# Optimization experiments

Measured on AMD Instinct MI355X. Metric: run time of the kernel, lower is better.

## Reference

```python
import jax, jax.numpy as jnp
import numpy as np
import math

EMB, HEADS, LATENT, FFN = 1024, 16, 256, 4096
HEAD_DIM = EMB // HEADS
B, N = 2, 2048
EPS = 1e-5


def _layer_norm(x, g, b):
    m = jnp.mean(x, axis=-1, keepdims=True)
    v = jnp.mean(jnp.square(x - m), axis=-1, keepdims=True)
    return (x - m) * jax.lax.rsqrt(v + EPS) * g + b


def setup_inputs() -> dict:
    key = jax.random.key(0)
    ks = jax.random.split(key, 20)
    s = 0.02
    def w(k, shape):
        return jax.random.normal(k, shape, dtype=jnp.float32) * s
    return {
        "x": jax.random.normal(ks[0], (B, N, EMB), dtype=jnp.float32),
        "attn_bias": jax.random.normal(ks[1], (N, N), dtype=jnp.float32),
        "Wq_w": w(ks[2], (EMB, EMB)),   "Wq_b": jnp.zeros((EMB,), jnp.float32),
        "WaK_w": w(ks[3], (EMB, LATENT)), "WaK_b": jnp.zeros((LATENT,), jnp.float32),
        "WbK_w": w(ks[4], (LATENT, EMB)), "WbK_b": jnp.zeros((EMB,), jnp.float32),
        "WaV_w": w(ks[5], (EMB, LATENT)), "WaV_b": jnp.zeros((LATENT,), jnp.float32),
        "WbV_w": w(ks[6], (LATENT, EMB)), "WbV_b": jnp.zeros((EMB,), jnp.float32),
        "Wo_w": w(ks[7], (EMB, EMB)),   "Wo_b": jnp.zeros((EMB,), jnp.float32),
        "ffn1_w": w(ks[8], (EMB, FFN)), "ffn1_b": jnp.zeros((FFN,), jnp.float32),
        "ffn2_w": w(ks[9], (FFN, EMB)), "ffn2_b": jnp.zeros((EMB,), jnp.float32),
        "ln1_g": jnp.ones((EMB,), jnp.float32), "ln1_b": jnp.zeros((EMB,), jnp.float32),
        "ln2_g": jnp.ones((EMB,), jnp.float32), "ln2_b": jnp.zeros((EMB,), jnp.float32),
    }


def reference(x, attn_bias, Wq_w, Wq_b, WaK_w, WaK_b, WbK_w, WbK_b,
              WaV_w, WaV_b, WbV_w, WbV_b, Wo_w, Wo_b,
              ffn1_w, ffn1_b, ffn2_w, ffn2_b, ln1_g, ln1_b, ln2_g, ln2_b):
    b, n, _ = x.shape
    Q = x @ Wq_w + Wq_b                                   # [B,N,E]
    K = (x @ WaK_w + WaK_b) @ WbK_w + WbK_b               # low-rank K
    V = (x @ WaV_w + WaV_b) @ WbV_w + WbV_b               # low-rank V
    Qh = Q.reshape(b, n, HEADS, HEAD_DIM)
    Kh = K.reshape(b, n, HEADS, HEAD_DIM)
    Vh = V.reshape(b, n, HEADS, HEAD_DIM)
    scale = 1.0 / math.sqrt(HEAD_DIM)
    scores = jnp.einsum('bnhd,bmhd->bhnm', Qh, Kh) * scale
    scores = scores + attn_bias[None, None, :, :]
    weights = jax.nn.softmax(scores, axis=-1)
    O = jnp.einsum('bhnm,bmhd->bnhd', weights, Vh).reshape(b, n, EMB)
    O = O @ Wo_w + Wo_b
    x1 = _layer_norm(x + O, ln1_g, ln1_b)
    h = jax.nn.gelu(x1 @ ffn1_w + ffn1_b, approximate=False)
    ffn_out = h @ ffn2_w + ffn2_b
    return _layer_norm(x1 + ffn_out, ln2_g, ln2_b)
```

## Files before the change

### kernel.cpp

```cpp
#include <hip/hip_runtime.h>
#include <hip/hip_bf16.h>
#include <math.h>

typedef __attribute__((ext_vector_type(4))) float f32x4;
typedef __attribute__((ext_vector_type(8))) __bf16 bf16x8;
typedef unsigned short u16;

#define L2E 1.44269504088896f

__device__ __forceinline__ u16 f2b(float f) {
  union { float f; unsigned u; } x; x.f = f;
  unsigned r = x.u + 0x7fffu + ((x.u >> 16) & 1u);
  return (u16)(r >> 16);
}

__device__ __forceinline__ void gl_lds16(const void* g, void* l) {
  __builtin_amdgcn_global_load_lds(
      (const __attribute__((address_space(1))) void*)g,
      (__attribute__((address_space(3))) void*)l, 16, 0, 0);
}

template<int EPI, int BN, int SPLITK>
__global__ __launch_bounds__(256, 3)
void gemm_bt(const u16* __restrict__ A, int lda,
             const u16* __restrict__ Bt,
             const float* __restrict__ bias,
             void* __restrict__ C, void* __restrict__ C2, int ldc,
             int M, int N, int K)
{
  constexpr int NF = BN / 32;
  __shared__ u16 As[128 * 32];
  __shared__ u16 Bs[BN * 32];
  const int t = threadIdx.x;
  const int lane = t & 63;
  const int w = t >> 6;
  const int wr = w >> 1, wc = w & 1;
  const int row0 = blockIdx.y * 128, col0 = blockIdx.x * BN;
  const int r = lane & 15, g = lane >> 4;

  f32x4 acc[4][NF];
#pragma unroll
  for (int m = 0; m < 4; ++m)
#pragma unroll
    for (int n = 0; n < NF; ++n) acc[m][n] = (f32x4){0.f, 0.f, 0.f, 0.f};

  const int KS = K / SPLITK;
  const int kbeg = (SPLITK > 1) ? blockIdx.z * KS : 0;

  const u16* Ag = A + (size_t)(row0 + (t >> 2)) * lda + (t & 3) * 8 + kbeg;
  const u16* Bg = Bt + (size_t)(col0 + (t >> 2)) * K + (t & 3) * 8 + kbeg;
  u16* Asw  = &As[t * 8];
  u16* Asw2 = &As[(t + 256) * 8];
  u16* Bsw  = &Bs[t * 8];
  u16* Bsw2 = (BN == 128) ? &Bs[(t + 256) * 8] : nullptr;
  const size_t a2 = (size_t)64 * lda, bo2 = (size_t)64 * K;

  for (int kt = 0; kt < KS; kt += 32) {
    gl_lds16(Ag + kt, Asw);
    gl_lds16(Ag + a2 + kt, Asw2);
    gl_lds16(Bg + kt, Bsw);
    if constexpr (BN == 128) gl_lds16(Bg + bo2 + kt, Bsw2);
    __syncthreads();
    bf16x8 af[4], bfr[NF];
#pragma unroll
    for (int m = 0; m < 4; ++m)
      af[m] = *(const bf16x8*)&As[(wr * 64 + m * 16 + r) * 32 + g * 8];
#pragma unroll
    for (int n = 0; n < NF; ++n)
      bfr[n] = *(const bf16x8*)&Bs[(wc * (BN / 2) + n * 16 + r) * 32 + g * 8];
#pragma unroll
    for (int m = 0; m < 4; ++m)
#pragma unroll
      for (int n = 0; n < NF; ++n)
        acc[m][n] = __builtin_amdgcn_mfma_f32_16x16x32_bf16(af[m], bfr[n], acc[m][n], 0, 0, 0);
    __syncthreads();
  }

  bool addb = true;
  float* Cf = (float*)C;
  if constexpr (SPLITK > 1) {
    if (blockIdx.z != 0) { addb = false; Cf = (float*)C2; }
  }

#pragma unroll
  for (int n = 0; n < NF; ++n) {
    const int col = col0 + wc * (BN / 2) + n * 16 + r;
    const float bv = addb ? bias[col] : 0.f;
#pragma unroll
    for (int m = 0; m < 4; ++m) {
      const int rb = row0 + wr * 64 + m * 16 + g * 4;
      if constexpr (EPI == 3) {
        const int b_ = rb >> 11, nn = rb & 2047;
        const int h_ = col >> 6, d_ = col & 63;
        u16* vp = (u16*)C + ((size_t)((b_ * 16 + h_) * 64 + d_)) * 2048 + nn;
        ushort4 pk;
        pk.x = f2b(acc[m][n][0] + bv);
        pk.y = f2b(acc[m][n][1] + bv);
        pk.z = f2b(acc[m][n][2] + bv);
        pk.w = f2b(acc[m][n][3] + bv);
        *(ushort4*)vp = pk;
      } else {
#pragma unroll
        for (int j = 0; j < 4; ++j) {
          float v = acc[m][n][j] + bv;
          if constexpr (EPI == 1) v = 0.5f * v * (1.0f + erff(v * 0.70710678118654752f));
          const size_t idx = (size_t)(rb + j) * ldc + col;
          if constexpr (EPI == 2) Cf[idx] = v;
          else ((u16*)C)[idx] = f2b(v);
        }
      }
    }
  }
}

__global__ __launch_bounds__(256, 4)
void attn_kernel(const u16* __restrict__ Qg,
                 const u16* __restrict__ Kg,
                 const u16* __restrict__ Vt,
                 const float* __restrict__ Bf,
                 u16* __restrict__ O)
{
  const int bh = blockIdx.x;
  const int b = bh >> 4, h = bh & 15;
  const int q0 = blockIdx.y * 64;
  const int t = threadIdx.x;
  const int lane = t & 63;
  const int w = t >> 6;
  const int r = lane & 15, g = lane >> 4;

  __shared__ u16 Ks[64 * 64];
  __shared__ u16 Vs[64 * 64];
  __shared__ __bf16 Ps[4][16 * 64];

  bf16x8 qa[2];
  {
    const size_t qrow = (size_t)(b * 2048 + q0 + w * 16 + r);
    const u16* qp = Qg + qrow * 1536 + h * 64 + g * 8;
    qa[0] = *(const bf16x8*)qp;
    qa[1] = *(const bf16x8*)(qp + 32);
#pragma unroll
    for (int dh = 0; dh < 2; ++dh)
#pragma unroll
      for (int i = 0; i < 8; ++i)
        qa[dh][i] = (__bf16)((float)qa[dh][i] * (0.125f * L2E));
  }

  f32x4 Oa[4];
#pragma unroll
  for (int dc = 0; dc < 4; ++dc) Oa[dc] = (f32x4){0.f, 0.f, 0.f, 0.f};
  float lsum[4] = {0.f, 0.f, 0.f, 0.f};

  const int srow = t >> 3;
  const int spos = t & 7;
  const int sseg  = spos ^ (srow & 7);
  const int srow2 = srow + 32;
  const int sseg2 = spos ^ (srow2 & 7);

  const float* bp = Bf + (size_t)(q0 + w * 16 + g * 4) * 2048 + r;

  for (int mt = 0; mt < 32; ++mt) {
    const int m0 = mt * 64;
    gl_lds16(Kg + (size_t)(b * 2048 + m0 + srow)  * 1024 + h * 64 + sseg * 8,  &Ks[t * 8]);
    gl_lds16(Kg + (size_t)(b * 2048 + m0 + srow2) * 1024 + h * 64 + sseg2 * 8, &Ks[(t + 256) * 8]);
    gl_lds16(Vt + (size_t)(bh * 64 + srow)  * 2048 + m0 + sseg * 8,  &Vs[t * 8]);
    gl_lds16(Vt + (size_t)(bh * 64 + srow2) * 2048 + m0 + sseg2 * 8, &Vs[(t + 256) * 8]);

    f32x4 s[4];
#pragma unroll
    for (int mc = 0; mc < 4; ++mc)
#pragma unroll
      for (int j = 0; j < 4; ++j)
        s[mc][j] = bp[(size_t)j * 2048 + m0 + mc * 16] * L2E;

    __syncthreads();

#pragma unroll
    for (int mc = 0; mc < 4; ++mc) {
      const int mrow = mc * 16 + r;
      const bf16x8 kb0 = *(const bf16x8*)&Ks[mrow * 64 + (((0 * 4 + g) ^ (mrow & 7)) * 8)];
      const bf16x8 kb1 = *(const bf16x8*)&Ks[mrow * 64 + (((1 * 4 + g) ^ (mrow & 7)) * 8)];
      s[mc] = __builtin_amdgcn_mfma_f32_16x16x32_bf16(qa[0], kb0, s[mc], 0, 0, 0);
      s[mc] = __builtin_amdgcn_mfma_f32_16x16x32_bf16(qa[1], kb1, s[mc], 0, 0, 0);
    }

    __bf16* pw = (__bf16*)Ps[w];
#pragma unroll
    for (int mc = 0; mc < 4; ++mc) {
      const int mm = mc * 16 + r;
#pragma unroll
      for (int j = 0; j < 4; ++j) {
        const float p = __builtin_amdgcn_exp2f(s[mc][j]);
        lsum[j] += p;
        const int qr = g * 4 + j;
        pw[qr * 64 + (((mm >> 3) ^ (qr & 7)) * 8) + (mm & 7)] = (__bf16)p;
      }
    }

    const bf16x8 pa0 = *(const bf16x8*)&pw[r * 64 + (((0 * 4 + g) ^ (r & 7)) * 8)];
    const bf16x8 pa1 = *(const bf16x8*)&pw[r * 64 + (((1 * 4 + g) ^ (r & 7)) * 8)];
#pragma unroll
    for (int dc = 0; dc < 4; ++dc) {
      const int drow = dc * 16 + r;
      const bf16x8 vb0 = *(const bf16x8*)&Vs[drow * 64 + (((0 * 4 + g) ^ (drow & 7)) * 8)];
      const bf16x8 vb1 = *(const bf16x8*)&Vs[drow * 64 + (((1 * 4 + g) ^ (drow & 7)) * 8)];
      Oa[dc] = __builtin_amdgcn_mfma_f32_16x16x32_bf16(pa0, vb0, Oa[dc], 0, 0, 0);
      Oa[dc] = __builtin_amdgcn_mfma_f32_16x16x32_bf16(pa1, vb1, Oa[dc], 0, 0, 0);
    }
    __syncthreads();
  }

#pragma unroll
  for (int off = 1; off < 16; off <<= 1)
#pragma unroll
    for (int j = 0; j < 4; ++j) lsum[j] += __shfl_xor(lsum[j], off);

  u16* Os = Ks;
#pragma unroll
  for (int j = 0; j < 4; ++j) {
    const float inv = 1.0f / lsum[j];
    const int qr = w * 16 + g * 4 + j;
#pragma unroll
    for (int dc = 0; dc < 4; ++dc)
      Os[qr * 64 + dc * 16 + r] = f2b(Oa[dc][j] * inv);
  }
  __syncthreads();
#pragma unroll
  for (int i = 0; i < 2; ++i) {
    const int tt = t + i * 256;
    const int orow = tt >> 3, oseg = tt & 7;
    const uint4 v = *(const uint4*)&Os[orow * 64 + oseg * 8];
    *(uint4*)&O[(size_t)(b * 2048 + q0 + orow) * 1024 + h * 64 + oseg * 8] = v;
  }
}

__global__ __launch_bounds__(256)
void prep_weights(const float* __restrict__ Wq, const float* __restrict__ WaK,
                  const float* __restrict__ WaV, const float* __restrict__ WbK,
                  const float* __restrict__ WbV, const float* __restrict__ Wo,
                  const float* __restrict__ F1, const float* __restrict__ F2,
                  u16* __restrict__ WB1, u16* __restrict__ WbKT,
                  u16* __restrict__ WbVT, u16* __restrict__ WoT,
                  u16* __restrict__ F1T, u16* __restrict__ F2T)
{
  const int bid = blockIdx.x;
  const float* src; u16* dst; int R, C, tile, tilesX;
  if (bid < 1024)      { src = Wq;  dst = WB1;             R = 1024; C = 1024; tile = bid;        tilesX = 32; }
  else if (bid < 1280) { src = WaK; dst = WB1 + 1024*1024; R = 1024; C = 256;  tile = bid - 1024; tilesX = 8; }
  else if (bid < 1536) { src = WaV; dst = WB1 + 1280*1024; R = 1024; C = 256;  tile = bid - 1280; tilesX = 8; }
  else if (bid < 1792) { src = WbK; dst = WbKT;            R = 256;  C = 1024; tile = bid - 1536; tilesX = 32; }
  else if (bid < 2048) { src = WbV; dst = WbVT;            R = 256;  C = 1024; tile = bid - 1792; tilesX = 32; }
  else if (bid < 3072) { src = Wo;  dst = WoT;             R = 1024; C = 1024; tile = bid - 2048; tilesX = 32; }
  else if (bid < 7168) { src = F1;  dst = F1T;             R = 1024; C = 4096; tile = bid - 3072; tilesX = 128; }
  else                 { src = F2;  dst = F2T;             R = 4096; C = 1024; tile = bid - 7168; tilesX = 32; }
  const int bx = tile % tilesX, by = tile / tilesX;
  const int c0 = bx * 32, r0 = by * 32;

  __shared__ float tl[32][33];
  const int tx = threadIdx.x, ty = threadIdx.y;
#pragma unroll
  for (int i = 0; i < 4; ++i)
    tl[ty + i * 8][tx] = src[(size_t)(r0 + ty + i * 8) * C + c0 + tx];
  __syncthreads();
#pragma unroll
  for (int i = 0; i < 4; ++i)
    dst[(size_t)(c0 + ty + i * 8) * R + r0 + tx] = f2b(tl[tx][ty + i * 8]);
}

__global__ void cvt_f32_bf16(const float* __restrict__ in, u16* __restrict__ out, int n4)
{
  const int i = blockIdx.x * 256 + threadIdx.x;
  if (i >= n4) return;
  const float4 v = ((const float4*)in)[i];
  ushort4 o;
  o.x = f2b(v.x); o.y = f2b(v.y); o.z = f2b(v.z); o.w = f2b(v.w);
  ((ushort4*)out)[i] = o;
}

__global__ void concat_bias(const float* __restrict__ a, const float* __restrict__ b,
                            const float* __restrict__ c, float* __restrict__ o)
{
  const int i = blockIdx.x * 256 + threadIdx.x;
  if (i < 1024) o[i] = a[i];
  else if (i < 1280) o[i] = b[i - 1024];
  else if (i < 1536) o[i] = c[i - 1280];
}

template<int WB, int NP>
__global__ __launch_bounds__(256)
void ln_kernel(const float* __restrict__ xa, const float* __restrict__ y0,
               const float* __restrict__ y1,
               const float* __restrict__ gam, const float* __restrict__ bet,
               float* __restrict__ outf, u16* __restrict__ outb)
{
  const int row = blockIdx.x, t = threadIdx.x;
  const float4 a = ((const float4*)(xa + (size_t)row * 1024))[t];
  const float4 c = ((const float4*)(y0 + (size_t)row * 1024))[t];
  float v0 = a.x + c.x, v1 = a.y + c.y, v2 = a.z + c.z, v3 = a.w + c.w;
  if constexpr (NP == 2) {
    const float4 d = ((const float4*)(y1 + (size_t)row * 1024))[t];
    v0 += d.x; v1 += d.y; v2 += d.z; v3 += d.w;
  }
  float s = v0 + v1 + v2 + v3;
  float q = v0 * v0 + v1 * v1 + v2 * v2 + v3 * v3;
#pragma unroll
  for (int off = 1; off < 64; off <<= 1) {
    s += __shfl_xor(s, off);
    q += __shfl_xor(q, off);
  }
  __shared__ float ss[4], qs[4];
  const int w = t >> 6, lane = t & 63;
  if (lane == 0) { ss[w] = s; qs[w] = q; }
  __syncthreads();
  const float S = ss[0] + ss[1] + ss[2] + ss[3];
  const float Q = qs[0] + qs[1] + qs[2] + qs[3];
  const float mean = S * (1.0f / 1024.0f);
  const float var = Q * (1.0f / 1024.0f) - mean * mean;
  const float rstd = rsqrtf(var + 1e-5f);
  const float4 gm = ((const float4*)gam)[t];
  const float4 bt = ((const float4*)bet)[t];
  const float o0 = (v0 - mean) * rstd * gm.x + bt.x;
  const float o1 = (v1 - mean) * rstd * gm.y + bt.y;
  const float o2 = (v2 - mean) * rstd * gm.z + bt.z;
  const float o3 = (v3 - mean) * rstd * gm.w + bt.w;
  float4 ov; ov.x = o0; ov.y = o1; ov.z = o2; ov.w = o3;
  ((float4*)(outf + (size_t)row * 1024))[t] = ov;
  if constexpr (WB) {
    ushort4 ob; ob.x = f2b(o0); ob.y = f2b(o1); ob.z = f2b(o2); ob.w = f2b(o3);
    ((ushort4*)(outb + (size_t)row * 1024))[t] = ob;
  }
}

extern "C" void kernel_launch(void* const* d_in, const int* in_sizes, int n_in,
                              void* d_out, int out_size, void* d_ws, size_t ws_size,
                              hipStream_t stream)
{
  const float* x     = (const float*)d_in[0];
  const float* abias = (const float*)d_in[1];
  const float* Wq_w  = (const float*)d_in[2];
  const float* Wq_b  = (const float*)d_in[3];
  const float* WaK_w = (const float*)d_in[4];
  const float* WaK_b = (const float*)d_in[5];
  const float* WbK_w = (const float*)d_in[6];
  const float* WbK_b = (const float*)d_in[7];
  const float* WaV_w = (const float*)d_in[8];
  const float* WaV_b = (const float*)d_in[9];
  const float* WbV_w = (const float*)d_in[10];
  const float* WbV_b = (const float*)d_in[11];
  const float* Wo_w  = (const float*)d_in[12];
  const float* Wo_b  = (const float*)d_in[13];
  const float* f1_w  = (const float*)d_in[14];
  const float* f1_b  = (const float*)d_in[15];
  const float* f2_w  = (const float*)d_in[16];
  const float* f2_b  = (const float*)d_in[17];
  const float* ln1_g = (const float*)d_in[18];
  const float* ln1_b = (const float*)d_in[19];
  const float* ln2_g = (const float*)d_in[20];
  const float* ln2_b = (const float*)d_in[21];

  char* ws = (char*)d_ws;
  u16*   xb    = (u16*)(ws + 0);
  u16*   WB1   = (u16*)(ws + 8388608);
  u16*   WbKT  = (u16*)(ws + 11534336);
  u16*   WbVT  = (u16*)(ws + 12058624);
  u16*   WoT   = (u16*)(ws + 12582912);
  u16*   F1T   = (u16*)(ws + 14680064);
  u16*   F2T   = (u16*)(ws + 23068672);
  float* bias1 = (float*)(ws + 31457280);
  u16*   G1    = (u16*)(ws + 39854080);
  u16*   Kb    = (u16*)(ws + 52436992);
  u16*   Vt    = (u16*)(ws + 60825600);
  u16*   Ob    = (u16*)(ws + 69214208);
  float* Y     = (float*)(ws + 77602816);
  float* x1f   = (float*)(ws + 94380032);
  u16*   x1b   = (u16*)(ws + 111157248);
  u16*   hbuf  = G1;
  float* Y1    = (float*)(ws + 0);

  prep_weights<<<11264, dim3(32, 8), 0, stream>>>(Wq_w, WaK_w, WaV_w, WbK_w, WbV_w,
                                                  Wo_w, f1_w, f2_w,
                                                  WB1, WbKT, WbVT, WoT, F1T, F2T);
  cvt_f32_bf16<<<4096, 256, 0, stream>>>(x, xb, 1048576);
  concat_bias<<<6, 256, 0, stream>>>(Wq_b, WaK_b, WaV_b, bias1);

  gemm_bt<0, 128, 1><<<dim3(12, 32), 256, 0, stream>>>(xb, 1024, WB1, bias1, G1, nullptr, 1536, 4096, 1536, 1024);
  gemm_bt<0, 64, 1><<<dim3(16, 32), 256, 0, stream>>>(G1 + 1024, 1536, WbKT, WbK_b, Kb, nullptr, 1024, 4096, 1024, 256);
  gemm_bt<3, 64, 1><<<dim3(16, 32), 256, 0, stream>>>(G1 + 1280, 1536, WbVT, WbV_b, Vt, nullptr, 2048, 4096, 1024, 256);
  attn_kernel<<<dim3(32, 32), 256, 0, stream>>>(G1, Kb, Vt, abias, Ob);
  gemm_bt<2, 64, 1><<<dim3(16, 32), 256, 0, stream>>>(Ob, 1024, WoT, Wo_b, Y, nullptr, 1024, 4096, 1024, 1024);
  ln_kernel<1, 1><<<4096, 256, 0, stream>>>(x, Y, Y, ln1_g, ln1_b, x1f, x1b);
  gemm_bt<1, 128, 1><<<dim3(32, 32), 256, 0, stream>>>(x1b, 1024, F1T, f1_b, hbuf, nullptr, 4096, 4096, 4096, 1024);
  gemm_bt<2, 128, 2><<<dim3(8, 32, 2), 256, 0, stream>>>(hbuf, 4096, F2T, f2_b, Y, Y1, 1024, 4096, 1024, 4096);
  ln_kernel<0, 2><<<4096, 256, 0, stream>>>(x1f, Y, Y1, ln2_g, ln2_b, (float*)d_out, nullptr);
}
```

Before: 417.7 us.

## Shrink attention blocks, prefetch bias tile into registers, raise MFMA priority

The attention kernel now runs 128-thread blocks that each cover 32 query rows, so the grid has twice as many blocks and more of them can be resident for latency hiding. The attn_bias values for the next key tile are loaded into registers during the current iteration instead of just before the QK MFMAs. s_setprio is raised around the MFMA sections. In exchange, every K/V tile is fetched into LDS by twice as many blocks, which raises global/L2 traffic and the per-block staging overhead.

Measured after the change: 425.4 us. No clear change (+1.8%).

```diff
diff --git a/kernel.cpp b/kernel.cpp
--- a/kernel.cpp
+++ b/kernel.cpp
@@ -113,7 +113,7 @@
   }
 }
 
-__global__ __launch_bounds__(256, 4)
+__global__ __launch_bounds__(128, 4)
 void attn_kernel(const u16* __restrict__ Qg,
                  const u16* __restrict__ Kg,
                  const u16* __restrict__ Vt,
@@ -122,7 +122,7 @@
 {
   const int bh = blockIdx.x;
   const int b = bh >> 4, h = bh & 15;
-  const int q0 = blockIdx.y * 64;
+  const int q0 = blockIdx.y * 32;
   const int t = threadIdx.x;
   const int lane = t & 63;
   const int w = t >> 6;
@@ -130,7 +130,7 @@
 
   __shared__ u16 Ks[64 * 64];
   __shared__ u16 Vs[64 * 64];
-  __shared__ __bf16 Ps[4][16 * 64];
+  __shared__ __bf16 Ps[2][16 * 64];
 
   bf16x8 qa[2];
   {
@@ -150,30 +150,48 @@
   for (int dc = 0; dc < 4; ++dc) Oa[dc] = (f32x4){0.f, 0.f, 0.f, 0.f};
   float lsum[4] = {0.f, 0.f, 0.f, 0.f};
 
-  const int srow = t >> 3;
-  const int spos = t & 7;
-  const int sseg  = spos ^ (srow & 7);
-  const int srow2 = srow + 32;
-  const int sseg2 = spos ^ (srow2 & 7);
+  int srw[4], ssg[4];
+#pragma unroll
+  for (int i = 0; i < 4; ++i) {
+    const int s_ = i * 128 + t;
+    srw[i] = s_ >> 3;
+    ssg[i] = (s_ & 7) ^ (srw[i] & 7);
+  }
+  const u16* Kb4[4];
+  const u16* Vb4[4];
+#pragma unroll
+  for (int i = 0; i < 4; ++i) {
+    Kb4[i] = Kg + (size_t)(b * 2048 + srw[i]) * 1024 + h * 64 + ssg[i] * 8;
+    Vb4[i] = Vt + (size_t)(bh * 64 + srw[i]) * 2048 + ssg[i] * 8;
+  }
 
   const float* bp = Bf + (size_t)(q0 + w * 16 + g * 4) * 2048 + r;
+
+  float bn[4][4];
+#pragma unroll
+  for (int mc = 0; mc < 4; ++mc)
+#pragma unroll
+    for (int j = 0; j < 4; ++j)
+      bn[mc][j] = bp[(size_t)j * 2048 + mc * 16];
 
   for (int mt = 0; mt < 32; ++mt) {
     const int m0 = mt * 64;
-    gl_lds16(Kg + (size_t)(b * 2048 + m0 + srow)  * 1024 + h * 64 + sseg * 8,  &Ks[t * 8]);
-    gl_lds16(Kg + (size_t)(b * 2048 + m0 + srow2) * 1024 + h * 64 + sseg2 * 8, &Ks[(t + 256) * 8]);
-    gl_lds16(Vt + (size_t)(bh * 64 + srow)  * 2048 + m0 + sseg * 8,  &Vs[t * 8]);
-    gl_lds16(Vt + (size_t)(bh * 64 + srow2) * 2048 + m0 + sseg2 * 8, &Vs[(t + 256) * 8]);
+#pragma unroll
+    for (int i = 0; i < 4; ++i) {
+      gl_lds16(Kb4[i] + (size_t)m0 * 1024, &Ks[(i * 128 + t) * 8]);
+      gl_lds16(Vb4[i] + m0, &Vs[(i * 128 + t) * 8]);
+    }
 
     f32x4 s[4];
 #pragma unroll
     for (int mc = 0; mc < 4; ++mc)
 #pragma unroll
       for (int j = 0; j < 4; ++j)
-        s[mc][j] = bp[(size_t)j * 2048 + m0 + mc * 16] * L2E;
+        s[mc][j] = bn[mc][j] * L2E;
 
     __syncthreads();
 
+    __builtin_amdgcn_s_setprio(1);
 #pragma unroll
     for (int mc = 0; mc < 4; ++mc) {
       const int mrow = mc * 16 + r;
@@ -182,6 +200,15 @@
       s[mc] = __builtin_amdgcn_mfma_f32_16x16x32_bf16(qa[0], kb0, s[mc], 0, 0, 0);
       s[mc] = __builtin_amdgcn_mfma_f32_16x16x32_bf16(qa[1], kb1, s[mc], 0, 0, 0);
     }
+    __builtin_amdgcn_s_setprio(0);
+
+    if (mt < 31) {
+#pragma unroll
+      for (int mc = 0; mc < 4; ++mc)
+#pragma unroll
+        for (int j = 0; j < 4; ++j)
+          bn[mc][j] = bp[(size_t)j * 2048 + (m0 + 64) + mc * 16];
+    }
 
     __bf16* pw = (__bf16*)Ps[w];
 #pragma unroll
@@ -198,6 +225,7 @@
 
     const bf16x8 pa0 = *(const bf16x8*)&pw[r * 64 + (((0 * 4 + g) ^ (r & 7)) * 8)];
     const bf16x8 pa1 = *(const bf16x8*)&pw[r * 64 + (((1 * 4 + g) ^ (r & 7)) * 8)];
+    __builtin_amdgcn_s_setprio(1);
 #pragma unroll
     for (int dc = 0; dc < 4; ++dc) {
       const int drow = dc * 16 + r;
@@ -206,6 +234,7 @@
       Oa[dc] = __builtin_amdgcn_mfma_f32_16x16x32_bf16(pa0, vb0, Oa[dc], 0, 0, 0);
       Oa[dc] = __builtin_amdgcn_mfma_f32_16x16x32_bf16(pa1, vb1, Oa[dc], 0, 0, 0);
     }
+    __builtin_amdgcn_s_setprio(0);
     __syncthreads();
   }
 
@@ -226,7 +255,7 @@
   __syncthreads();
 #pragma unroll
   for (int i = 0; i < 2; ++i) {
-    const int tt = t + i * 256;
+    const int tt = t + i * 128;
     const int orow = tt >> 3, oseg = tt & 7;
     const uint4 v = *(const uint4*)&Os[orow * 64 + oseg * 8];
     *(uint4*)&O[(size_t)(b * 2048 + q0 + orow) * 1024 + h * 64 + oseg * 8] = v;
@@ -385,7 +414,7 @@
   gemm_bt<0, 128, 1><<<dim3(12, 32), 256, 0, stream>>>(xb, 1024, WB1, bias1, G1, nullptr, 1536, 4096, 1536, 1024);
   gemm_bt<0, 64, 1><<<dim3(16, 32), 256, 0, stream>>>(G1 + 1024, 1536, WbKT, WbK_b, Kb, nullptr, 1024, 4096, 1024, 256);
   gemm_bt<3, 64, 1><<<dim3(16, 32), 256, 0, stream>>>(G1 + 1280, 1536, WbVT, WbV_b, Vt, nullptr, 2048, 4096, 1024, 256);
-  attn_kernel<<<dim3(32, 32), 256, 0, stream>>>(G1, Kb, Vt, abias, Ob);
+  attn_kernel<<<dim3(32, 64), 128, 0, stream>>>(G1, Kb, Vt, abias, Ob);
   gemm_bt<2, 64, 1><<<dim3(16, 32), 256, 0, stream>>>(Ob, 1024, WoT, Wo_b, Y, nullptr, 1024, 4096, 1024, 1024);
   ln_kernel<1, 1><<<4096, 256, 0, stream>>>(x, Y, Y, ln1_g, ln1_b, x1f, x1b);
   gemm_bt<1, 128, 1><<<dim3(32, 32), 256, 0, stream>>>(x1b, 1024, F1T, f1_b, hbuf, nullptr, 4096, 4096, 4096, 1024);
```

## Double-buffer LDS tiles in GEMM and attention loops, prefetch bias, raise MFMA priority

Applied to the files above, without the earlier changes.

Both the GEMM and the attention kernels now keep two LDS buffers. The loads for the next K or KV tile are issued before computing on the current one, so each iteration has one barrier instead of stalling on a load before every compute step. The attention kernel also loads the next tile's bias values into registers during the current iteration. MFMA sections are wrapped in s_setprio. LDS use per block doubles for the K/V and A/B tiles, which may limit occupancy. This matters most for the attention kernel, which is already near the LDS limit at 4 blocks per CU.

Result: no change. 418.2 us (+0.1%).

```diff
diff --git a/kernel.cpp b/kernel.cpp
--- a/kernel.cpp
+++ b/kernel.cpp
@@ -29,8 +29,8 @@
              int M, int N, int K)
 {
   constexpr int NF = BN / 32;
-  __shared__ u16 As[128 * 32];
-  __shared__ u16 Bs[BN * 32];
+  __shared__ u16 As[2][128 * 32];
+  __shared__ u16 Bs[2][BN * 32];
   const int t = threadIdx.x;
   const int lane = t & 63;
   const int w = t >> 6;
@@ -49,31 +49,40 @@
 
   const u16* Ag = A + (size_t)(row0 + (t >> 2)) * lda + (t & 3) * 8 + kbeg;
   const u16* Bg = Bt + (size_t)(col0 + (t >> 2)) * K + (t & 3) * 8 + kbeg;
-  u16* Asw  = &As[t * 8];
-  u16* Asw2 = &As[(t + 256) * 8];
-  u16* Bsw  = &Bs[t * 8];
-  u16* Bsw2 = (BN == 128) ? &Bs[(t + 256) * 8] : nullptr;
   const size_t a2 = (size_t)64 * lda, bo2 = (size_t)64 * K;
-
+  const int si0 = t * 8, si1 = (t + 256) * 8;
+
+  gl_lds16(Ag, &As[0][si0]);
+  gl_lds16(Ag + a2, &As[0][si1]);
+  gl_lds16(Bg, &Bs[0][si0]);
+  if constexpr (BN == 128) gl_lds16(Bg + bo2, &Bs[0][si1]);
+  __syncthreads();
+
+  int buf = 0;
   for (int kt = 0; kt < KS; kt += 32) {
-    gl_lds16(Ag + kt, Asw);
-    gl_lds16(Ag + a2 + kt, Asw2);
-    gl_lds16(Bg + kt, Bsw);
-    if constexpr (BN == 128) gl_lds16(Bg + bo2 + kt, Bsw2);
-    __syncthreads();
+    const int kn = kt + 32;
+    if (kn < KS) {
+      gl_lds16(Ag + kn, &As[buf ^ 1][si0]);
+      gl_lds16(Ag + a2 + kn, &As[buf ^ 1][si1]);
+      gl_lds16(Bg + kn, &Bs[buf ^ 1][si0]);
+      if constexpr (BN == 128) gl_lds16(Bg + bo2 + kn, &Bs[buf ^ 1][si1]);
+    }
     bf16x8 af[4], bfr[NF];
 #pragma unroll
     for (int m = 0; m < 4; ++m)
-      af[m] = *(const bf16x8*)&As[(wr * 64 + m * 16 + r) * 32 + g * 8];
+      af[m] = *(const bf16x8*)&As[buf][(wr * 64 + m * 16 + r) * 32 + g * 8];
 #pragma unroll
     for (int n = 0; n < NF; ++n)
-      bfr[n] = *(const bf16x8*)&Bs[(wc * (BN / 2) + n * 16 + r) * 32 + g * 8];
+      bfr[n] = *(const bf16x8*)&Bs[buf][(wc * (BN / 2) + n * 16 + r) * 32 + g * 8];
+    __builtin_amdgcn_s_setprio(1);
 #pragma unroll
     for (int m = 0; m < 4; ++m)
 #pragma unroll
       for (int n = 0; n < NF; ++n)
         acc[m][n] = __builtin_amdgcn_mfma_f32_16x16x32_bf16(af[m], bfr[n], acc[m][n], 0, 0, 0);
+    __builtin_amdgcn_s_setprio(0);
     __syncthreads();
+    buf ^= 1;
   }
 
   bool addb = true;
@@ -128,8 +137,8 @@
   const int w = t >> 6;
   const int r = lane & 15, g = lane >> 4;
 
-  __shared__ u16 Ks[64 * 64];
-  __shared__ u16 Vs[64 * 64];
+  __shared__ u16 Ks[2][64 * 64];
+  __shared__ u16 Vs[2][64 * 64];
   __shared__ __bf16 Ps[4][16 * 64];
 
   bf16x8 qa[2];
@@ -155,32 +164,63 @@
   const int sseg  = spos ^ (srow & 7);
   const int srow2 = srow + 32;
   const int sseg2 = spos ^ (srow2 & 7);
+  const int si0 = t * 8, si1 = (t + 256) * 8;
+
+  const u16* Kp0 = Kg + (size_t)(b * 2048 + srow)  * 1024 + h * 64 + sseg * 8;
+  const u16* Kp1 = Kg + (size_t)(b * 2048 + srow2) * 1024 + h * 64 + sseg2 * 8;
+  const u16* Vp0 = Vt + (size_t)(bh * 64 + srow)  * 2048 + sseg * 8;
+  const u16* Vp1 = Vt + (size_t)(bh * 64 + srow2) * 2048 + sseg2 * 8;
 
   const float* bp = Bf + (size_t)(q0 + w * 16 + g * 4) * 2048 + r;
 
+  float bn[4][4];
+#pragma unroll
+  for (int mc = 0; mc < 4; ++mc)
+#pragma unroll
+    for (int j = 0; j < 4; ++j)
+      bn[mc][j] = bp[(size_t)j * 2048 + mc * 16];
+
+  gl_lds16(Kp0, &Ks[0][si0]);
+  gl_lds16(Kp1, &Ks[0][si1]);
+  gl_lds16(Vp0, &Vs[0][si0]);
+  gl_lds16(Vp1, &Vs[0][si1]);
+  __syncthreads();
+
+  int buf = 0;
   for (int mt = 0; mt < 32; ++mt) {
     const int m0 = mt * 64;
-    gl_lds16(Kg + (size_t)(b * 2048 + m0 + srow)  * 1024 + h * 64 + sseg * 8,  &Ks[t * 8]);
-    gl_lds16(Kg + (size_t)(b * 2048 + m0 + srow2) * 1024 + h * 64 + sseg2 * 8, &Ks[(t + 256) * 8]);
-    gl_lds16(Vt + (size_t)(bh * 64 + srow)  * 2048 + m0 + sseg * 8,  &Vs[t * 8]);
-    gl_lds16(Vt + (size_t)(bh * 64 + srow2) * 2048 + m0 + sseg2 * 8, &Vs[(t + 256) * 8]);
+    if (mt < 31) {
+      const int mn = m0 + 64;
+      gl_lds16(Kp0 + (size_t)mn * 1024, &Ks[buf ^ 1][si0]);
+      gl_lds16(Kp1 + (size_t)mn * 1024, &Ks[buf ^ 1][si1]);
+      gl_lds16(Vp0 + mn, &Vs[buf ^ 1][si0]);
+      gl_lds16(Vp1 + mn, &Vs[buf ^ 1][si1]);
+    }
 
     f32x4 s[4];
 #pragma unroll
     for (int mc = 0; mc < 4; ++mc)
 #pragma unroll
       for (int j = 0; j < 4; ++j)
-        s[mc][j] = bp[(size_t)j * 2048 + m0 + mc * 16] * L2E;
-
-    __syncthreads();
-
+        s[mc][j] = bn[mc][j] * L2E;
+
+    __builtin_amdgcn_s_setprio(1);
 #pragma unroll
     for (int mc = 0; mc < 4; ++mc) {
       const int mrow = mc * 16 + r;
-      const bf16x8 kb0 = *(const bf16x8*)&Ks[mrow * 64 + (((0 * 4 + g) ^ (mrow & 7)) * 8)];
-      const bf16x8 kb1 = *(const bf16x8*)&Ks[mrow * 64 + (((1 * 4 + g) ^ (mrow & 7)) * 8)];
+      const bf16x8 kb0 = *(const bf16x8*)&Ks[buf][mrow * 64 + (((0 * 4 + g) ^ (mrow & 7)) * 8)];
+      const bf16x8 kb1 = *(const bf16x8*)&Ks[buf][mrow * 64 + (((1 * 4 + g) ^ (mrow & 7)) * 8)];
       s[mc] = __builtin_amdgcn_mfma_f32_16x16x32_bf16(qa[0], kb0, s[mc], 0, 0, 0);
       s[mc] = __builtin_amdgcn_mfma_f32_16x16x32_bf16(qa[1], kb1, s[mc], 0, 0, 0);
+    }
+    __builtin_amdgcn_s_setprio(0);
+
+    if (mt < 31) {
+#pragma unroll
+      for (int mc = 0; mc < 4; ++mc)
+#pragma unroll
+        for (int j = 0; j < 4; ++j)
+          bn[mc][j] = bp[(size_t)j * 2048 + (m0 + 64) + mc * 16];
     }
 
     __bf16* pw = (__bf16*)Ps[w];
@@ -198,15 +238,18 @@
 
     const bf16x8 pa0 = *(const bf16x8*)&pw[r * 64 + (((0 * 4 + g) ^ (r & 7)) * 8)];
     const bf16x8 pa1 = *(const bf16x8*)&pw[r * 64 + (((1 * 4 + g) ^ (r & 7)) * 8)];
+    __builtin_amdgcn_s_setprio(1);
 #pragma unroll
     for (int dc = 0; dc < 4; ++dc) {
       const int drow = dc * 16 + r;
-      const bf16x8 vb0 = *(const bf16x8*)&Vs[drow * 64 + (((0 * 4 + g) ^ (drow & 7)) * 8)];
-      const bf16x8 vb1 = *(const bf16x8*)&Vs[drow * 64 + (((1 * 4 + g) ^ (drow & 7)) * 8)];
+      const bf16x8 vb0 = *(const bf16x8*)&Vs[buf][drow * 64 + (((0 * 4 + g) ^ (drow & 7)) * 8)];
+      const bf16x8 vb1 = *(const bf16x8*)&Vs[buf][drow * 64 + (((1 * 4 + g) ^ (drow & 7)) * 8)];
       Oa[dc] = __builtin_amdgcn_mfma_f32_16x16x32_bf16(pa0, vb0, Oa[dc], 0, 0, 0);
       Oa[dc] = __builtin_amdgcn_mfma_f32_16x16x32_bf16(pa1, vb1, Oa[dc], 0, 0, 0);
     }
+    __builtin_amdgcn_s_setprio(0);
     __syncthreads();
+    buf ^= 1;
   }
 
 #pragma unroll
@@ -214,7 +257,7 @@
 #pragma unroll
     for (int j = 0; j < 4; ++j) lsum[j] += __shfl_xor(lsum[j], off);
 
-  u16* Os = Ks;
+  u16* Os = Ks[0];
 #pragma unroll
   for (int j = 0; j < 4; ++j) {
     const float inv = 1.0f / lsum[j];
```
